# Kernel tuning notes

Hardware: AMD Instinct MI355X
Metric: run time of the kernel (lower is better)

The kernel has to match this reference:

```python
import jax, jax.numpy as jnp
import numpy as np

E = 512      # embedding_dim == head_dim
H = 8        # num_heads
F = E * H    # ffn_dim = 4096
B = 2
S = 2048
SCALE = float(np.sqrt(E))


def setup_inputs() -> dict:
    key = jax.random.key(0)
    kx, kq, kk, kv, ko = jax.random.split(key, 5)
    x = jax.random.normal(kx, (B, S, E), dtype=jnp.float32)
    # torch Linear weights: [out_features, in_features], y = x @ W.T
    w_std = 1.0 / np.sqrt(E)
    Wq = jax.random.normal(kq, (F, E), dtype=jnp.float32) * w_std
    Wk = jax.random.normal(kk, (F, E), dtype=jnp.float32) * w_std
    Wv = jax.random.normal(kv, (F, E), dtype=jnp.float32) * w_std
    Wo = jax.random.normal(ko, (E, F), dtype=jnp.float32) * (1.0 / np.sqrt(F))
    # causal mask: 1 where attended, 0 where masked (masked_fill(mask == 0, -inf))
    attn_mask = jnp.tril(jnp.ones((S, S), dtype=jnp.int32))[None, None]  # [1,1,S,S]
    return {"x": x, "attn_mask": attn_mask, "Wq": Wq, "Wk": Wk, "Wv": Wv, "Wo": Wo}


def reference(x, attn_mask, Wq, Wk, Wv, Wo):
    b, s, _ = x.shape
    # projections + split heads: [B,S,F] -> [B,S,H,E]
    q = (x @ Wq.T).reshape(b, s, H, E)
    k = (x @ Wk.T).reshape(b, s, H, E)
    v = (x @ Wv.T).reshape(b, s, H, E)
    # scaled dot-product scores [B,H,S,S]
    scores = jnp.einsum('bqhd,bkhd->bhqk', q, k) / SCALE
    scores = jnp.where(attn_mask == 0, -jnp.inf, scores)
    w = jax.nn.softmax(scores, axis=-1)
    # dropout rate 0.0 (eval) -> identity
    out = jnp.einsum('bhqk,bkhd->bqhd', w, v).reshape(b, s, F)
    return out @ Wo.T  # [B,S,E]
```

## Files before the change

### kernel.cpp

```cpp
#include <hip/hip_runtime.h>
#include <hip/hip_bf16.h>

typedef __attribute__((ext_vector_type(8))) short short8;
typedef __attribute__((ext_vector_type(4))) float f32x4;
typedef __attribute__((ext_vector_type(8))) unsigned short ushort8;

#define LDS_ASYNC16(gsrc, ldst) \
  __builtin_amdgcn_global_load_lds((const __attribute__((address_space(1))) void*)(gsrc), \
                                   (__attribute__((address_space(3))) void*)(ldst), 16, 0, 0)

__device__ __forceinline__ unsigned short f2bf(float f) {
  unsigned int u = __float_as_uint(f);
  unsigned int r = (u + 0x7FFFu + ((u >> 16) & 1u)) >> 16;
  return (unsigned short)r;
}
__device__ __forceinline__ float bf2f(unsigned short h) {
  return __uint_as_float((unsigned int)h << 16);
}

__global__ __launch_bounds__(256) void cast5_f32_bf16(
    const float* __restrict__ i0, const float* __restrict__ i1, const float* __restrict__ i2,
    const float* __restrict__ i3, const float* __restrict__ i4,
    unsigned short* __restrict__ out) {
  const float* src[5] = {i0, i1, i2, i3, i4};
  int z = blockIdx.z;
  const float* in = src[z];
  size_t i = ((size_t)blockIdx.x * 256 + threadIdx.x) * 8;
  float4 a = *(const float4*)(in + i);
  float4 b = *(const float4*)(in + i + 4);
  ushort8 o;
  o[0] = f2bf(a.x); o[1] = f2bf(a.y); o[2] = f2bf(a.z); o[3] = f2bf(a.w);
  o[4] = f2bf(b.x); o[5] = f2bf(b.y); o[6] = f2bf(b.z); o[7] = f2bf(b.w);
  *(ushort8*)(out + (size_t)z * 2097152 + i) = o;
}

__global__ __launch_bounds__(256) void transpose_v(const unsigned short* __restrict__ V,
                                                   unsigned short* __restrict__ Vt) {
  __shared__ unsigned short t[64][72];
  int slot = blockIdx.z;
  int k0 = blockIdx.x << 6, d0 = blockIdx.y << 6;
  const unsigned short* src = V + (size_t)k0 * 4096 + slot * 512 + d0;
  int rr = threadIdx.x >> 3;
  int cc = (threadIdx.x & 7) << 3;
#pragma unroll
  for (int half = 0; half < 64; half += 32) {
    int r = rr + half;
    ushort8 v = *(const ushort8*)(src + (size_t)r * 4096 + cc);
#pragma unroll
    for (int e = 0; e < 8; ++e) t[cc + e][r] = v[e];
  }
  __syncthreads();
  unsigned short* dst = Vt + ((size_t)slot * 512 + d0) * 2048 + k0;
#pragma unroll
  for (int half = 0; half < 64; half += 32) {
    int d = rr + half;
    *(ushort8*)(dst + (size_t)d * 2048 + cc) = *(const ushort8*)&t[d][cc];
  }
}

__global__ __launch_bounds__(256) void softmax_causal_bf16(unsigned short* __restrict__ S) {
  int row = blockIdx.x;
  int q = row & 2047;
  unsigned short* srow = S + (size_t)row * 2048;
  int n = q + 1;
  int nW = ((q >> 7) + 1) << 7;
  int t = threadIdx.x, wave = t >> 6, lane = t & 63;
  int base = t * 8;
  ushort8 u = {};
  if (base < nW) u = *(const ushort8*)(srow + base);
  float vals[8];
  float m = -1e30f;
#pragma unroll
  for (int e = 0; e < 8; ++e) {
    float v = bf2f(u[e]);
    vals[e] = (base + e < n) ? v : -1e30f;
    m = fmaxf(m, vals[e]);
  }
#pragma unroll
  for (int off = 32; off > 0; off >>= 1) m = fmaxf(m, __shfl_xor(m, off, 64));
  __shared__ float red[8];
  if (lane == 0) red[wave] = m;
  __syncthreads();
  m = fmaxf(fmaxf(red[0], red[1]), fmaxf(red[2], red[3]));
  float s = 0.f;
#pragma unroll
  for (int e = 0; e < 8; ++e) {
    float ex = (base + e < n) ? __expf(vals[e] - m) : 0.f;
    vals[e] = ex; s += ex;
  }
#pragma unroll
  for (int off = 32; off > 0; off >>= 1) s += __shfl_xor(s, off, 64);
  if (lane == 0) red[4 + wave] = s;
  __syncthreads();
  s = red[4] + red[5] + red[6] + red[7];
  float inv = 1.0f / s;
  if (base < nW) {
    ushort8 o;
#pragma unroll
    for (int e = 0; e < 8; ++e) o[e] = f2bf(vals[e] * inv);
    *(ushort8*)(srow + base) = o;
  }
}

__global__ __launch_bounds__(256) void reduce_k4(const float4* __restrict__ p,
                                                 float4* __restrict__ out, int n4) {
  int i = blockIdx.x * 256 + threadIdx.x;
  if (i >= n4) return;
  float4 a = p[i], b = p[i + n4], c = p[i + 2 * n4], d = p[i + 3 * n4];
  float4 o;
  o.x = (a.x + b.x) + (c.x + d.x);
  o.y = (a.y + b.y) + (c.y + d.y);
  o.z = (a.z + b.z) + (c.z + d.z);
  o.w = (a.w + b.w) + (c.w + d.w);
  out[i] = o;
}

#define STGU(u_)                                                                   \
  do {                                                                             \
    int kb_ = (u_) * 32;                                                           \
    unsigned short* Ad_ = AsBase + ((u_) & 3) * 8192 + tid * 8;                    \
    unsigned short* Bd_ = BsBase + ((u_) & 3) * 8192 + tid * 8;                    \
    LDS_ASYNC16(Ap + (size_t)(m0 + r0) * lda + kb_ + cs0, Ad_);                    \
    LDS_ASYNC16(Bp + (size_t)(n0 + r0) * ldb + kb_ + cs0, Bd_);                    \
    LDS_ASYNC16(Ap + (size_t)(m0 + r0 + 128) * lda + kb_ + cs0, Ad_ + 4096);       \
    LDS_ASYNC16(Bp + (size_t)(n0 + r0 + 128) * ldb + kb_ + cs0, Bd_ + 4096);       \
  } while (0)

#define RDFR(u_, AF, BF)                                                           \
  {                                                                                \
    const unsigned short* Au_ = AsBase + ((u_) & 3) * 8192;                        \
    const unsigned short* Bu_ = BsBase + ((u_) & 3) * 8192;                        \
    _Pragma("unroll") for (int j_ = 0; j_ < 8; ++j_)                               \
      AF[j_] = *(const short8*)(Au_ + (wm * 128 + j_ * 16 + lr) * 32 + sA);        \
    _Pragma("unroll") for (int j_ = 0; j_ < 4; ++j_)                               \
      BF[j_] = *(const short8*)(Bu_ + (wn * 64 + j_ * 16 + lr) * 32 + sA);         \
  }

#define MMAC(AF, BF)                                                               \
  __builtin_amdgcn_s_setprio(1);                                                   \
  _Pragma("unroll") for (int j_ = 0; j_ < 8; ++j_)                                 \
    _Pragma("unroll") for (int j2_ = 0; j2_ < 4; ++j2_)                            \
      acc[j_][j2_] = __builtin_amdgcn_mfma_f32_16x16x32_bf16(AF[j_], BF[j2_],      \
                                                             acc[j_][j2_], 0, 0, 0); \
  __builtin_amdgcn_s_setprio(0);

#define VMC4() asm volatile("s_waitcnt vmcnt(4)" ::: "memory")
#define VMC0() asm volatile("s_waitcnt vmcnt(0)" ::: "memory")
#define VMC8() asm volatile("s_waitcnt vmcnt(8)" ::: "memory")
#define BARR() __builtin_amdgcn_s_barrier()

template<int OUT_F32, int CSKIP>
__global__ __launch_bounds__(512, 2) void gemm8p(
    const unsigned short* __restrict__ A, const unsigned short* __restrict__ B,
    void* __restrict__ C, int K , int lda, int ldb, int ldc, int nH,
    long long sAb, long long sAh, long long sBb, long long sBh,
    long long sCb, long long sCh, float scale)
{
  __shared__ unsigned short AsBase[4 * 8192];
  __shared__ unsigned short BsBase[4 * 8192];
  int bx = blockIdx.x, by = blockIdx.y;
  if (CSKIP) {
    int t = bx;
    int ty = (int)((sqrtf(8.0f * (float)t + 1.0f) - 1.0f) * 0.5f);
    while ((ty + 1) * (ty + 2) / 2 <= t) ++ty;
    while (ty * (ty + 1) / 2 > t) --ty;
    bx = t - ty * (ty + 1) / 2;
    by = ty;
  }
  int m0 = by * 256, n0 = bx * 256;
  int z = blockIdx.z;
  int zb = z / nH, zh = z - zb * nH;
  const unsigned short* Ap = A + (size_t)(zb * sAb + zh * sAh);
  const unsigned short* Bp = B + (size_t)(zb * sBb + zh * sBh);
  size_t coff = (size_t)(zb * sCb + zh * sCh);
  int tid = threadIdx.x;
  int wid = tid >> 6, lane = tid & 63;
  int wm = wid >> 2, wn = wid & 3;
  int lr = lane & 15, hi = lane >> 4;
  int sA  = (hi ^ ((lr >> 1) & 3)) << 3;
  int r0  = tid >> 2;
  int cs0 = ((tid & 3) ^ ((r0 >> 1) & 3)) << 3;

  short8 af0[8], bf0[4], af1[8], bf1[4];
  f32x4 acc[8][4] = {};

  STGU(0); STGU(1); STGU(2);
  VMC8(); BARR();
  RDFR(0, af0, bf0);
  VMC4(); BARR();

  for (int u = 0; u < 12; u += 2) {
    RDFR(u + 1, af1, bf1); STGU(u + 3); MMAC(af0, bf0); VMC4(); BARR();
    RDFR(u + 2, af0, bf0); STGU(u + 4); MMAC(af1, bf1); VMC4(); BARR();
  }
  RDFR(13, af1, bf1); STGU(15); MMAC(af0, bf0); VMC4(); BARR();
  RDFR(14, af0, bf0);           MMAC(af1, bf1); VMC0(); BARR();
  RDFR(15, af1, bf1);           MMAC(af0, bf0);         BARR();
                                MMAC(af1, bf1);

#pragma unroll
  for (int m = 0; m < 8; ++m)
#pragma unroll
    for (int n = 0; n < 4; ++n)
#pragma unroll
      for (int r = 0; r < 4; ++r) {
        int row = m0 + wm * 128 + m * 16 + hi * 4 + r;
        int col = n0 + wn * 64 + n * 16 + lr;
        float v = acc[m][n][r] * scale;
        if (OUT_F32) ((float*)C)[coff + (size_t)row * ldc + col] = v;
        else ((unsigned short*)C)[coff + (size_t)row * ldc + col] = f2bf(v);
      }
}

template<int OUT_F32, int CSKIP, int KCLIP>
__global__ __launch_bounds__(256, 2) void gemm_bt(
    const unsigned short* __restrict__ A, const unsigned short* __restrict__ B,
    void* __restrict__ C, int K, int lda, int ldb, int ldc, int nH,
    long long sAb, long long sAh, long long sBb, long long sBh,
    long long sCb, long long sCh, float scale)
{
  __shared__ unsigned short As[128 * 64];
  __shared__ unsigned short Bs[128 * 64];
  int m0 = blockIdx.y * 128, n0 = blockIdx.x * 128;
  if (CSKIP && n0 > m0) return;
  int z = blockIdx.z;
  int zb = z / nH, zh = z - zb * nH;
  const unsigned short* Ap = A + (size_t)(zb * sAb + zh * sAh);
  const unsigned short* Bp = B + (size_t)(zb * sBb + zh * sBh);
  size_t coff = (size_t)(zb * sCb + zh * sCh);
  int tid = threadIdx.x;
  int wave = tid >> 6, lane = tid & 63;
  int kEnd = KCLIP ? min(K, m0 + 128) : K;

  int wr = (wave >> 1) * 64, wc = (wave & 1) * 64;
  int lr = lane & 15;
  int lkb = (lane >> 4) * 8;

  f32x4 acc[4][4] = {};

  for (int k0 = 0; k0 < kEnd; k0 += 64) {
#pragma unroll
    for (int it = 0; it < 4; ++it) {
      int g = it * 256 + tid;
      int r = g >> 3, c = (g & 7) << 3;
      LDS_ASYNC16(Ap + (size_t)(m0 + r) * lda + (k0 + c), As + (size_t)(it * 256 + wave * 64) * 8);
      LDS_ASYNC16(Bp + (size_t)(n0 + r) * ldb + (k0 + c), Bs + (size_t)(it * 256 + wave * 64) * 8);
    }
    __syncthreads();
#pragma unroll
    for (int kk = 0; kk < 64; kk += 32) {
      short8 a[4], b[4];
#pragma unroll
      for (int i = 0; i < 4; ++i)
        a[i] = *(const short8*)(As + (size_t)(wr + i * 16 + lr) * 64 + kk + lkb);
#pragma unroll
      for (int j = 0; j < 4; ++j)
        b[j] = *(const short8*)(Bs + (size_t)(wc + j * 16 + lr) * 64 + kk + lkb);
#pragma unroll
      for (int i = 0; i < 4; ++i)
#pragma unroll
        for (int j = 0; j < 4; ++j)
          acc[i][j] = __builtin_amdgcn_mfma_f32_16x16x32_bf16(a[i], b[j], acc[i][j], 0, 0, 0);
    }
    __syncthreads();
  }

  int orow = (lane >> 4) * 4, ocol = lane & 15;
#pragma unroll
  for (int i = 0; i < 4; ++i)
#pragma unroll
    for (int j = 0; j < 4; ++j)
#pragma unroll
      for (int r = 0; r < 4; ++r) {
        int row = m0 + wr + i * 16 + orow + r;
        int col = n0 + wc + j * 16 + ocol;
        float v = acc[i][j][r] * scale;
        if (OUT_F32) ((float*)C)[coff + (size_t)row * ldc + col] = v;
        else ((unsigned short*)C)[coff + (size_t)row * ldc + col] = f2bf(v);
      }
}

extern "C" void kernel_launch(void* const* d_in, const int* in_sizes, int n_in,
                              void* d_out, int out_size, void* d_ws, size_t ws_size,
                              hipStream_t stream) {
  const float* x  = (const float*)d_in[0];
  const float* Wq = (const float*)d_in[2];
  const float* Wk = (const float*)d_in[3];
  const float* Wv = (const float*)d_in[4];
  const float* Wo = (const float*)d_in[5];

  if (ws_size < (size_t)188 * (1 << 20)) return;

  char* ws = (char*)d_ws;
  unsigned short* xb   = (unsigned short*)(ws);
  unsigned short* Wob  = (unsigned short*)(ws + (size_t)16  * (1 << 20));
  unsigned short* QKV  = (unsigned short*)(ws + (size_t)20  * (1 << 20));
  unsigned short* Sc   = (unsigned short*)(ws + (size_t)116 * (1 << 20));
  unsigned short* Vt   = (unsigned short*)(ws);
  float*          Pp   = (float*)(ws + (size_t)116 * (1 << 20));

  const int NEw = 4096 * 512;
  const long long NEm = 4096LL * 4096;

  cast5_f32_bf16<<<dim3(1024, 1, 5), 256, 0, stream>>>(x, Wq, Wk, Wv, Wo, xb);

  gemm8p<0, 0><<<dim3(16, 16, 3), 512, 0, stream>>>(
      xb, xb + NEw, QKV, 512, 512, 512, 4096, 3,
      0LL, 0LL, 0LL, (long long)NEw, 0LL, NEm, 1.0f);

  for (int b = 0; b < 2; ++b) {
    size_t tokOff = (size_t)b * 2048 * 4096;
    const unsigned short* Qb = QKV + tokOff;
    const unsigned short* Kb = QKV + NEm + tokOff;
    const unsigned short* Vb = QKV + 2 * NEm + tokOff;
    unsigned short* AOb = QKV + tokOff;

    gemm8p<0, 1><<<dim3(36, 1, 8), 512, 0, stream>>>(
        Qb, Kb, Sc, 512, 4096, 4096, 2048, 8,
        0LL, 512LL, 0LL, 512LL, 0LL, 2048LL * 2048, 0.04419417382415922f);

    transpose_v<<<dim3(32, 8, 8), 256, 0, stream>>>(Vb, Vt);

    softmax_causal_bf16<<<dim3(8 * 2048), 256, 0, stream>>>(Sc);

    gemm_bt<0, 0, 1><<<dim3(4, 16, 8), 256, 0, stream>>>(
        Sc, Vt, AOb, 2048, 2048, 2048, 4096, 8,
        0LL, 2048LL * 2048, 0LL, 512LL * 2048, 0LL, 512LL, 1.0f);
  }

  gemm_bt<1, 0, 0><<<dim3(4, 32, 4), 256, 0, stream>>>(
      QKV, Wob, Pp, 1024, 4096, 4096, 512, 4,
      0LL, 1024LL, 0LL, 1024LL, 0LL, 2097152LL, 1.0f);

  reduce_k4<<<dim3(2048), 256, 0, stream>>>((const float4*)Pp, (float4*)d_out, 524288);
}
```

Baseline: 340.5 us.

## Split GEMM k-step into two half-phases interleaving LDS reads with MFMA

Restructures the 8-wave GEMM main loop so that each k-step runs in two phases: the upper half of the A fragments is read while the lower half is multiplied, then the next step's lower A and B fragments are read while the upper half is multiplied. Explicit lgkmcnt waits, sched_barriers and extra workgroup barriers order the phases. This shrinks fragment register use (four A fragments live instead of eight) and aims to hide LDS read latency behind MFMA work. The trade is roughly twice as many barriers per k-step, plus waitcnt bookkeeping that is tricky to get right in the tail of the loop.

```diff
diff --git a/kernel.cpp b/kernel.cpp
--- a/kernel.cpp
+++ b/kernel.cpp
@@ -126,28 +126,55 @@
     LDS_ASYNC16(Bp + (size_t)(n0 + r0 + 128) * ldb + kb_ + cs0, Bd_ + 4096);       \
   } while (0)
 
-#define RDFR(u_, AF, BF)                                                           \
-  {                                                                                \
-    const unsigned short* Au_ = AsBase + ((u_) & 3) * 8192;                        \
-    const unsigned short* Bu_ = BsBase + ((u_) & 3) * 8192;                        \
-    _Pragma("unroll") for (int j_ = 0; j_ < 8; ++j_)                               \
-      AF[j_] = *(const short8*)(Au_ + (wm * 128 + j_ * 16 + lr) * 32 + sA);        \
+#define RDA_LO(u_, AF)                                                             \
+  { const unsigned short* Au_ = AsBase + ((u_) & 3) * 8192;                        \
     _Pragma("unroll") for (int j_ = 0; j_ < 4; ++j_)                               \
-      BF[j_] = *(const short8*)(Bu_ + (wn * 64 + j_ * 16 + lr) * 32 + sA);         \
-  }
-
-#define MMAC(AF, BF)                                                               \
+      AF[j_] = *(const short8*)(Au_ + (wm * 128 + j_ * 16 + lr) * 32 + sA); }
+
+#define RDA_HI(u_, AF)                                                             \
+  { const unsigned short* Au_ = AsBase + ((u_) & 3) * 8192;                        \
+    _Pragma("unroll") for (int j_ = 0; j_ < 4; ++j_)                               \
+      AF[j_] = *(const short8*)(Au_ + (wm * 128 + (4 + j_) * 16 + lr) * 32 + sA); }
+
+#define RDB4(u_, BF)                                                               \
+  { const unsigned short* Bu_ = BsBase + ((u_) & 3) * 8192;                        \
+    _Pragma("unroll") for (int j_ = 0; j_ < 4; ++j_)                               \
+      BF[j_] = *(const short8*)(Bu_ + (wn * 64 + j_ * 16 + lr) * 32 + sA); }
+
+#define LGKM(n_)                                                                   \
+  asm volatile("s_waitcnt lgkmcnt(" #n_ ")" ::: "memory");                         \
+  __builtin_amdgcn_sched_barrier(0)
+
+#define MM16(AF, RB, BF)                                                           \
   __builtin_amdgcn_s_setprio(1);                                                   \
-  _Pragma("unroll") for (int j_ = 0; j_ < 8; ++j_)                                 \
+  _Pragma("unroll") for (int j_ = 0; j_ < 4; ++j_)                                 \
     _Pragma("unroll") for (int j2_ = 0; j2_ < 4; ++j2_)                            \
-      acc[j_][j2_] = __builtin_amdgcn_mfma_f32_16x16x32_bf16(AF[j_], BF[j2_],      \
-                                                             acc[j_][j2_], 0, 0, 0); \
+      acc[(RB) + j_][j2_] = __builtin_amdgcn_mfma_f32_16x16x32_bf16(               \
+          AF[j_], BF[j2_], acc[(RB) + j_][j2_], 0, 0, 0);                          \
   __builtin_amdgcn_s_setprio(0);
 
 #define VMC4() asm volatile("s_waitcnt vmcnt(4)" ::: "memory")
 #define VMC0() asm volatile("s_waitcnt vmcnt(0)" ::: "memory")
 #define VMC8() asm volatile("s_waitcnt vmcnt(8)" ::: "memory")
 #define BARR() __builtin_amdgcn_s_barrier()
+
+#define SPA(u_, BBC, DOSTG)                                                        \
+  RDA_HI(u_, aHi);                                                                 \
+  if (DOSTG) STGU((u_) + 3);                                                       \
+  BARR(); LGKM(4);                                                                 \
+  MM16(aLo, 0, BBC);                                                               \
+  BARR();
+
+#define SPB(u_, BBN, BBC, WAITOP)                                                  \
+  RDA_LO((u_) + 1, aLo); RDB4((u_) + 1, BBN);                                      \
+  BARR(); LGKM(8);                                                                 \
+  MM16(aHi, 4, BBC);                                                               \
+  WAITOP; BARR();
+
+#define SPB_LAST(BBC)                                                              \
+  BARR(); LGKM(0);                                                                 \
+  MM16(aHi, 4, BBC);                                                               \
+  BARR();
 
 template<int OUT_F32, int CSKIP>
 __global__ __launch_bounds__(512, 2) void gemm8p(
@@ -181,22 +208,21 @@
   int r0  = tid >> 2;
   int cs0 = ((tid & 3) ^ ((r0 >> 1) & 3)) << 3;
 
-  short8 af0[8], bf0[4], af1[8], bf1[4];
+  short8 aLo[4], aHi[4], bb0[4], bb1[4];
   f32x4 acc[8][4] = {};
 
   STGU(0); STGU(1); STGU(2);
   VMC8(); BARR();
-  RDFR(0, af0, bf0);
-  VMC4(); BARR();
+  RDA_LO(0, aLo); RDB4(0, bb0);
 
   for (int u = 0; u < 12; u += 2) {
-    RDFR(u + 1, af1, bf1); STGU(u + 3); MMAC(af0, bf0); VMC4(); BARR();
-    RDFR(u + 2, af0, bf0); STGU(u + 4); MMAC(af1, bf1); VMC4(); BARR();
-  }
-  RDFR(13, af1, bf1); STGU(15); MMAC(af0, bf0); VMC4(); BARR();
-  RDFR(14, af0, bf0);           MMAC(af1, bf1); VMC0(); BARR();
-  RDFR(15, af1, bf1);           MMAC(af0, bf0);         BARR();
-                                MMAC(af1, bf1);
+    SPA(u, bb0, 1)      SPB(u, bb1, bb0, VMC8())
+    SPA(u + 1, bb1, 1)  SPB(u + 1, bb0, bb1, VMC8())
+  }
+  SPA(12, bb0, 1)  SPB(12, bb1, bb0, VMC8())
+  SPA(13, bb1, 0)  SPB(13, bb0, bb1, VMC4())
+  SPA(14, bb0, 0)  SPB(14, bb1, bb0, VMC0())
+  SPA(15, bb1, 0)  SPB_LAST(bb1)
 
 #pragma unroll
   for (int m = 0; m < 8; ++m)
```

Result: slower. 351.1 us (+3.1%).
